# Kernel tuning notes

Hardware: AMD Instinct MI355X
Metric: run time of the kernel (lower is better)

## Reference

```python
import jax, jax.numpy as jnp
import numpy as np

B, T, C = 2, 2048, 512
H = 16
HS = C // H  # 32
DF = 4 * C   # 2048
EPS = 1e-3   # keras LayerNormalization default


def setup_inputs() -> dict:
    key = jax.random.key(0)
    ks = jax.random.split(key, 16)
    s = 0.02
    return {
        "x":  jax.random.normal(ks[0], (B, T, C), jnp.float32),
        "Wq": jax.random.normal(ks[1], (H, C, HS), jnp.float32) * s,
        "bq": jnp.zeros((H, HS), jnp.float32),
        "Wk": jax.random.normal(ks[2], (H, C, HS), jnp.float32) * s,
        "bk": jnp.zeros((H, HS), jnp.float32),
        "Wv": jax.random.normal(ks[3], (H, C, HS), jnp.float32) * s,
        "bv": jnp.zeros((H, HS), jnp.float32),
        "Wo": jax.random.normal(ks[4], (C, C), jnp.float32) * s,
        "bo": jnp.zeros((C,), jnp.float32),
        "W1": jax.random.normal(ks[5], (C, DF), jnp.float32) * s,
        "b1": jnp.zeros((DF,), jnp.float32),
        "W2": jax.random.normal(ks[6], (DF, C), jnp.float32) * s,
        "b2": jnp.zeros((C,), jnp.float32),
        "g1": jnp.ones((C,), jnp.float32),
        "be1": jnp.zeros((C,), jnp.float32),
        "g2": jnp.ones((C,), jnp.float32),
        "be2": jnp.zeros((C,), jnp.float32),
    }


def _layernorm(x, g, b):
    mu = jnp.mean(x, axis=-1, keepdims=True)
    var = jnp.mean(jnp.square(x - mu), axis=-1, keepdims=True)
    return (x - mu) / jnp.sqrt(var + EPS) * g + b


def reference(x, Wq, bq, Wk, bk, Wv, bv, Wo, bo, W1, b1, W2, b2, g1, be1, g2, be2):
    Bx, Tx, Cx = x.shape
    # --- attention branch (pre-LN) ---
    h = _layernorm(x, g1, be1)
    q = jnp.einsum('btc,hcd->bhtd', h, Wq) + bq[None, :, None, :]
    k = jnp.einsum('btc,hcd->bhtd', h, Wk) + bk[None, :, None, :]
    v = jnp.einsum('btc,hcd->bhtd', h, Wv) + bv[None, :, None, :]
    # NOTE: source code never applies 1/sqrt(head_size) to scores (mask-only scaling bug)
    scores = jnp.einsum('bhtd,bhsd->bhts', q, k)           # [B,H,T,T]
    causal = jnp.tril(jnp.ones((Tx, Tx), dtype=bool))
    scores = jnp.where(causal, scores, -jnp.inf)
    att = jax.nn.softmax(scores, axis=-1)
    o = jnp.einsum('bhts,bhsd->bhtd', att, v)              # [B,H,T,HS]
    o = o.transpose(0, 2, 1, 3).reshape(Bx, Tx, Cx)        # concat heads
    x = x + o @ Wo + bo
    # --- FFN branch (pre-LN) ---
    h2 = _layernorm(x, g2, be2)
    f = jax.nn.relu(h2 @ W1 + b1) @ W2 + b2
    return x + f
```

## Files before the change

### kernel.cpp

```cpp
#include <hip/hip_runtime.h>
#include <hip/hip_bf16.h>

#define T_  2048
#define C_  512
#define H_  16
#define HS_ 32
#define DF_ 2048
#define B_  2
#define M_  4096

typedef __attribute__((ext_vector_type(8))) short short8;
typedef __attribute__((ext_vector_type(4))) short short4v;
typedef __attribute__((ext_vector_type(4))) float f32x4;
typedef __attribute__((ext_vector_type(16))) float f32x16;

__device__ inline short bf16r(float f) {
  union { float f; unsigned u; } v; v.f = f;
  return (short)((v.u + 0x7FFFu + ((v.u >> 16) & 1u)) >> 16);
}

__device__ inline f32x4 mfma16(short8 a, short8 b, f32x4 c) {
  return __builtin_amdgcn_mfma_f32_16x16x32_bf16(a, b, c, 0, 0, 0);
}
__device__ inline f32x16 mfma32(short8 a, short8 b, f32x16 c) {
  return __builtin_amdgcn_mfma_f32_32x32x16_bf16(a, b, c, 0, 0, 0);
}

__device__ inline unsigned cvtpk(float lo, float hi) {
  unsigned r;
  asm("v_cvt_pk_bf16_f32 %0, %1, %2" : "=v"(r) : "v"(lo), "v"(hi));
  return r;
}

__device__ inline void gload_lds16(const short* g, short* l) {
  __builtin_amdgcn_global_load_lds(
      (const __attribute__((address_space(1))) unsigned int*)g,
      (__attribute__((address_space(3))) unsigned int*)l, 16, 0, 0);
}

__device__ inline void ln_row(int row, const float* src, const float* g,
                              const float* be, short* dst, int lane) {
  const float* xr = src + (size_t)row * C_;
  float4 a = *(const float4*)(xr + lane * 8);
  float4 b = *(const float4*)(xr + lane * 8 + 4);
  float vals[8] = {a.x, a.y, a.z, a.w, b.x, b.y, b.z, b.w};
  float s = 0.f, ss = 0.f;
  #pragma unroll
  for (int i = 0; i < 8; ++i) { s += vals[i]; ss += vals[i] * vals[i]; }
  #pragma unroll
  for (int off = 1; off < 64; off <<= 1) {
    s += __shfl_xor(s, off);
    ss += __shfl_xor(ss, off);
  }
  float mu = s * (1.f / C_);
  float rstd = rsqrtf(ss * (1.f / C_) - mu * mu + 1e-3f);
  short8 o;
  #pragma unroll
  for (int i = 0; i < 8; ++i)
    o[i] = bf16r((vals[i] - mu) * rstd * g[lane * 8 + i] + be[lane * 8 + i]);
  *(short8*)(dst + (size_t)row * C_ + lane * 8) = o;
}

__global__ __launch_bounds__(256) void prep_kernel(
    const float* __restrict__ x, const float* __restrict__ g1, const float* __restrict__ be1,
    const float* __restrict__ Wq, const float* __restrict__ Wk, const float* __restrict__ Wv,
    const float* __restrict__ Wo, const float* __restrict__ W1, const float* __restrict__ W2,
    short* __restrict__ h1, short* __restrict__ Wqkv, short* __restrict__ Wop,
    short* __restrict__ W1p, short* __restrict__ W2p) {
  __shared__ float tile[32][33];
  int id = blockIdx.x;
  int tid = threadIdx.x;
  if (id >= 3072) {
    int w = tid >> 6, lane = tid & 63;
    ln_row((id - 3072) * 4 + w, x, g1, be1, h1, lane);
    return;
  }
  const float* src; short* dst;
  int srcN, dstK, k0, n0;
  size_t dstBase;
  if (id < 768) {
    int s = id >> 4, ct = id & 15;
    int proj = s >> 4, hh = s & 15;
    src = (proj == 0 ? Wq : (proj == 1 ? Wk : Wv)) + (size_t)hh * 512 * 32;
    srcN = 32; dstK = 512; k0 = ct * 32; n0 = 0;
    dst = Wqkv; dstBase = (size_t)(proj * 512 + hh * 32);
  } else if (id < 1024) {
    int t = id - 768;
    src = Wo; srcN = 512; dstK = 512;
    k0 = (t >> 4) * 32; n0 = (t & 15) * 32; dst = Wop; dstBase = 0;
  } else if (id < 2048) {
    int t = id - 1024;
    src = W1; srcN = 2048; dstK = 512;
    k0 = (t >> 6) * 32; n0 = (t & 63) * 32; dst = W1p; dstBase = 0;
  } else {
    int t = id - 2048;
    src = W2; srcN = 512; dstK = 2048;
    k0 = (t >> 4) * 32; n0 = (t & 15) * 32; dst = W2p; dstBase = 0;
  }
  int rr = tid >> 3, rc = (tid & 7) * 4;
  float4 v4 = *(const float4*)(src + (size_t)(k0 + rr) * srcN + n0 + rc);
  tile[rr][rc + 0] = v4.x; tile[rr][rc + 1] = v4.y;
  tile[rr][rc + 2] = v4.z; tile[rr][rc + 3] = v4.w;
  __syncthreads();
  int wn = tid >> 3, wk = (tid & 7) * 4;
  short4v o;
  o[0] = bf16r(tile[wk + 0][wn]);
  o[1] = bf16r(tile[wk + 1][wn]);
  o[2] = bf16r(tile[wk + 2][wn]);
  o[3] = bf16r(tile[wk + 3][wn]);
  *(short4v*)(dst + (dstBase + n0 + wn) * (size_t)dstK + k0 + wk) = o;
}

__global__ __launch_bounds__(256) void ln2_kernel(
    const float* __restrict__ x, const float* __restrict__ g, const float* __restrict__ be,
    short* __restrict__ out) {
  int w = threadIdx.x >> 6, lane = threadIdx.x & 63;
  ln_row(blockIdx.x * 4 + w, x, g, be, out, lane);
}

template<int BM, int BN, int WM, int WN, int KDIM, int FM, int FN>
__device__ inline void gemm_core(const short* __restrict__ A, const short* __restrict__ Bw,
                                 int m0, int n0, f32x4 (&acc)[FM][FN]) {
  static_assert(WM * WN == 4 && FM == BM / WM / 16 && FN == BN / WN / 16, "geometry");
  __shared__ short lA[2][BM * 64];
  __shared__ short lB[2][BN * 64];
  const int tid = threadIdx.x, w = tid >> 6, lane = tid & 63;
  const int cl = lane & 15, g = lane >> 4;
  const int wm = w / WN, wn = w % WN;
  const int srow = tid >> 3;
  const int sug  = (tid & 7) ^ (srow & 7);
  constexpr int NT = KDIM / 64;

  auto stage = [&](int buf, int k0) {
    #pragma unroll
    for (int j = 0; j < BM / 32; ++j)
      gload_lds16(A + (size_t)(m0 + j * 32 + srow) * KDIM + k0 + sug * 8,
                  &lA[buf][j * 2048 + tid * 8]);
    #pragma unroll
    for (int j = 0; j < BN / 32; ++j)
      gload_lds16(Bw + (size_t)(n0 + j * 32 + srow) * KDIM + k0 + sug * 8,
                  &lB[buf][j * 2048 + tid * 8]);
  };

  stage(0, 0);
  __syncthreads();
  int cur = 0;
  for (int t = 0; t < NT; ++t) {
    if (t + 1 < NT) stage(cur ^ 1, (t + 1) * 64);
    #pragma unroll
    for (int kk = 0; kk < 2; ++kk) {
      const int uswz = ((kk * 4 + g) ^ (cl & 7)) * 8;
      short8 a[FM], b[FN];
      #pragma unroll
      for (int mi = 0; mi < FM; ++mi)
        a[mi] = *(const short8*)&lA[cur][(wm * (BM / WM) + mi * 16 + cl) * 64 + uswz];
      #pragma unroll
      for (int ni = 0; ni < FN; ++ni)
        b[ni] = *(const short8*)&lB[cur][(wn * (BN / WN) + ni * 16 + cl) * 64 + uswz];
      #pragma unroll
      for (int mi = 0; mi < FM; ++mi)
        #pragma unroll
        for (int ni = 0; ni < FN; ++ni)
          acc[mi][ni] = mfma16(a[mi], b[ni], acc[mi][ni]);
    }
    __syncthreads();
    cur ^= 1;
  }
}

__global__ __launch_bounds__(256) void gemm_qkvt(
    const short* __restrict__ h1, const short* __restrict__ Wqkv,
    const float* __restrict__ bq, const float* __restrict__ bk,
    const float* __restrict__ bv,
    short* __restrict__ qb, short* __restrict__ kb, short* __restrict__ vTb) {
  int id = blockIdx.x;
  const short *Ap, *Bp;
  int m0, n0;
  bool isv = id >= 256;
  if (!isv) {
    int xcd = id & 7, s = id >> 3;
    m0 = (xcd * 4 + (s & 3)) * 128;
    n0 = (s >> 2) * 128;
    Ap = h1; Bp = Wqkv;
  } else {
    int t = id - 256;
    int xcd = t & 7, s = t >> 3;
    n0 = (xcd * 4 + (s & 3)) * 128;
    m0 = (s >> 2) * 128;
    Ap = Wqkv + 1024 * 512; Bp = h1;
  }
  f32x4 acc[4][4] = {};
  gemm_core<128, 128, 2, 2, 512, 4, 4>(Ap, Bp, m0, n0, acc);
  int w = threadIdx.x >> 6, lane = threadIdx.x & 63;
  int cl = lane & 15, rb = (lane >> 4) * 4;
  int wm = w >> 1, wn = w & 1;
  if (!isv) {
    #pragma unroll
    for (int mi = 0; mi < 4; ++mi)
      #pragma unroll
      for (int ni = 0; ni < 4; ++ni)
        #pragma unroll
        for (int r = 0; r < 4; ++r) {
          int mm = m0 + wm * 64 + mi * 16 + rb + r;
          int n  = n0 + wn * 64 + ni * 16 + cl;
          int proj = n >> 9, rem = n & 511;
          int hh = rem >> 5, d = rem & 31;
          int b = mm >> 11, t = mm & (T_ - 1);
          size_t bh = (size_t)b * H_ + hh;
          float val = acc[mi][ni][r];
          if (proj == 0) qb[(bh * T_ + t) * HS_ + d] = bf16r(val + bq[rem]);
          else           kb[(bh * T_ + t) * HS_ + d] = bf16r(val + bk[rem]);
        }
  } else {
    #pragma unroll
    for (int mi = 0; mi < 4; ++mi)
      #pragma unroll
      for (int ni = 0; ni < 4; ++ni)
        #pragma unroll
        for (int r = 0; r < 4; ++r) {
          int m = m0 + wm * 64 + mi * 16 + rb + r;
          int n = n0 + wn * 64 + ni * 16 + cl;
          vTb[(size_t)(n >> 11) * (512 * 2048) + (size_t)m * T_ + (n & 2047)] =
              bf16r(acc[mi][ni][r] + bv[m]);
        }
  }
}

__global__ __launch_bounds__(256) void gemm_out(
    const short* __restrict__ A, const short* __restrict__ W,
    const float* __restrict__ bo, const float* __restrict__ xres,
    float* __restrict__ x1) {
  int id = blockIdx.x;
  int xcd = id & 7, s = id >> 3;
  int m0 = (xcd * 8 + (s & 7)) * 64;
  int n0 = (s >> 3) * 64;
  f32x4 acc[2][2] = {};
  gemm_core<64, 64, 2, 2, 512, 2, 2>(A, W, m0, n0, acc);
  int w = threadIdx.x >> 6, lane = threadIdx.x & 63;
  int cl = lane & 15, rb = (lane >> 4) * 4;
  int wm = w >> 1, wn = w & 1;
  #pragma unroll
  for (int mi = 0; mi < 2; ++mi)
    #pragma unroll
    for (int ni = 0; ni < 2; ++ni)
      #pragma unroll
      for (int r = 0; r < 4; ++r) {
        int mm = m0 + wm * 32 + mi * 16 + rb + r;
        int n  = n0 + wn * 32 + ni * 16 + cl;
        x1[(size_t)mm * C_ + n] = acc[mi][ni][r] + bo[n] + xres[(size_t)mm * C_ + n];
      }
}

__global__ __launch_bounds__(256) void gemm_ffn1(
    const short* __restrict__ A, const short* __restrict__ W,
    const float* __restrict__ b1, short* __restrict__ f1) {
  int id = blockIdx.x;
  int xcd = id & 7, s = id >> 3;
  int m0 = (xcd * 4 + (s & 3)) * 128;
  int n0 = (s >> 2) * 128;
  f32x4 acc[4][4] = {};
  gemm_core<128, 128, 2, 2, 512, 4, 4>(A, W, m0, n0, acc);
  int w = threadIdx.x >> 6, lane = threadIdx.x & 63;
  int cl = lane & 15, rb = (lane >> 4) * 4;
  int wm = w >> 1, wn = w & 1;
  #pragma unroll
  for (int mi = 0; mi < 4; ++mi)
    #pragma unroll
    for (int ni = 0; ni < 4; ++ni)
      #pragma unroll
      for (int r = 0; r < 4; ++r) {
        int mm = m0 + wm * 64 + mi * 16 + rb + r;
        int n  = n0 + wn * 64 + ni * 16 + cl;
        f1[(size_t)mm * DF_ + n] = bf16r(fmaxf(acc[mi][ni][r] + b1[n], 0.f));
      }
}

__global__ __launch_bounds__(256) void gemm_ffn2(
    const short* __restrict__ A, const short* __restrict__ W,
    const float* __restrict__ b2, const float* __restrict__ x1,
    float* __restrict__ out) {
  int id = blockIdx.x;
  int xcd = id & 7, s = id >> 3;
  int m0 = (xcd * 8 + (s & 7)) * 64;
  int n0 = (s >> 3) * 64;
  f32x4 acc[2][2] = {};
  gemm_core<64, 64, 2, 2, 2048, 2, 2>(A, W, m0, n0, acc);
  int w = threadIdx.x >> 6, lane = threadIdx.x & 63;
  int cl = lane & 15, rb = (lane >> 4) * 4;
  int wm = w >> 1, wn = w & 1;
  #pragma unroll
  for (int mi = 0; mi < 2; ++mi)
    #pragma unroll
    for (int ni = 0; ni < 2; ++ni)
      #pragma unroll
      for (int r = 0; r < 4; ++r) {
        int mm = m0 + wm * 32 + mi * 16 + rb + r;
        int n  = n0 + wn * 32 + ni * 16 + cl;
        out[(size_t)mm * C_ + n] = acc[mi][ni][r] + b2[n] + x1[(size_t)mm * C_ + n];
      }
}

__global__ __launch_bounds__(256) void attn_kernel(
    const short* __restrict__ qb, const short* __restrict__ kb,
    const short* __restrict__ vTb, short* __restrict__ ob) {
  __shared__ float accbuf[4][64][17];
  __shared__ float lbuf[4][32];
  __shared__ short tbuf[32][34];
  const int id = blockIdx.x;
  const int xcd = id & 7, s = id >> 3;
  const int headin = s & 3;
  const int qt = 63 - (s >> 2);
  const int bh = xcd * 4 + headin;
  const int w = threadIdx.x >> 6, lane = threadIdx.x & 63;
  const int cl = lane & 31, g = lane >> 5;
  const int q0 = qt * 32, q = q0 + cl;
  const float L2E = 1.44269504f;
  const float NFM = -16.f * L2E;

  const short* Qp  = qb  + (size_t)bh * T_ * HS_;
  const short* Kp  = kb  + (size_t)bh * T_ * HS_;
  const short* VTp = vTb + (size_t)bh * HS_ * T_;

  const int nc   = qt + 1;
  const int cbeg = (nc * w) >> 2;
  const int cend = (nc * (w + 1)) >> 2;

  f32x16 acc = {};
  float l = 0.f;

  if (cbeg < cend) {
    short8 qf0 = *(const short8*)(Qp + (size_t)q * HS_ + g * 8);
    short8 qf1 = *(const short8*)(Qp + (size_t)q * HS_ + 16 + g * 8);
    const int kc0 = cbeg << 5;
    short8 ka  = *(const short8*)(Kp + (size_t)(kc0 + cl) * HS_ + g * 8);
    short8 kc2 = *(const short8*)(Kp + (size_t)(kc0 + cl) * HS_ + 16 + g * 8);
    short8 va  = *(const short8*)(VTp + (size_t)cl * T_ + kc0 + g * 8);
    short8 vb  = *(const short8*)(VTp + (size_t)cl * T_ + kc0 + 16 + g * 8);

    for (int c = cbeg; c < cend; ++c) {
      const int kc = c << 5;
      f32x16 Z = {};
      f32x16 S = mfma32(ka, qf0, Z);
      S = mfma32(kc2, qf1, S);

      short8 kan, kbn, van, vbn;
      if (c + 1 < cend) {
        const int kn = kc + 32;
        kan = *(const short8*)(Kp + (size_t)(kn + cl) * HS_ + g * 8);
        kbn = *(const short8*)(Kp + (size_t)(kn + cl) * HS_ + 16 + g * 8);
        van = *(const short8*)(VTp + (size_t)cl * T_ + kn + g * 8);
        vbn = *(const short8*)(VTp + (size_t)cl * T_ + kn + 16 + g * 8);
      }

      if (c == nc - 1) {
        #pragma unroll
        for (int r = 0; r < 16; ++r) {
          int key = kc + (r & 3) + 8 * (r >> 2) + 4 * g;
          if (key > q) S[r] = -1e30f;
        }
      }

      float p[16];
      #pragma unroll
      for (int r = 0; r < 16; ++r) p[r] = exp2f(fmaf(S[r], L2E, NFM));
      float sm[8];
      #pragma unroll
      for (int r = 0; r < 8; ++r) sm[r] = p[r] + p[r + 8];
      #pragma unroll
      for (int r = 0; r < 4; ++r) sm[r] += sm[r + 4];
      float ps = (sm[0] + sm[1]) + (sm[2] + sm[3]);
      ps += __shfl_xor(ps, 32);
      l += ps;

      #pragma unroll
      for (int sb = 0; sb < 2; ++sb) {
        unsigned L0 = cvtpk(p[sb * 8 + 0], p[sb * 8 + 1]);
        unsigned L1 = cvtpk(p[sb * 8 + 2], p[sb * 8 + 3]);
        unsigned H0 = cvtpk(p[sb * 8 + 4], p[sb * 8 + 5]);
        unsigned H1 = cvtpk(p[sb * 8 + 6], p[sb * 8 + 7]);
        auto r02 = __builtin_amdgcn_permlane32_swap(L0, H0, false, false);
        auto r13 = __builtin_amdgcn_permlane32_swap(L1, H1, false, false);
        union { unsigned u[4]; short8 v; } pb;
        pb.u[0] = r02[0]; pb.u[1] = r13[0]; pb.u[2] = r02[1]; pb.u[3] = r13[1];
        acc = mfma32(sb == 0 ? va : vb, pb.v, acc);
      }

      ka = kan; kc2 = kbn; va = van; vb = vbn;
    }
  }

  #pragma unroll
  for (int r = 0; r < 16; ++r) accbuf[w][lane][r] = acc[r];
  if (lane < 32) lbuf[w][cl] = l;
  __syncthreads();

  if (w == 0) {
    float lsum = lbuf[0][cl] + lbuf[1][cl] + lbuf[2][cl] + lbuf[3][cl];
    float inv = 1.f / lsum;
    #pragma unroll
    for (int r = 0; r < 16; ++r) {
      float v = accbuf[0][lane][r] + accbuf[1][lane][r] +
                accbuf[2][lane][r] + accbuf[3][lane][r];
      int d = (r & 3) + 8 * (r >> 2) + 4 * g;
      tbuf[cl][d] = bf16r(v * inv);
    }
  }
  __syncthreads();

  int qr = threadIdx.x >> 3, col = (threadIdx.x & 7) * 4;
  const int b = bh >> 4, hh = bh & 15;
  short4v o4;
  o4[0] = tbuf[qr][col + 0];
  o4[1] = tbuf[qr][col + 1];
  o4[2] = tbuf[qr][col + 2];
  o4[3] = tbuf[qr][col + 3];
  *(short4v*)(ob + ((size_t)b * T_ + q0 + qr) * C_ + hh * HS_ + col) = o4;
}

#define OFF_H1   ((size_t)0)
#define OFF_WQKV ((size_t)4194304)
#define OFF_WO   ((size_t)5767168)
#define OFF_W1   ((size_t)6291456)
#define OFF_W2   ((size_t)8388608)
#define OFF_Q    ((size_t)10485760)
#define OFF_K    ((size_t)14680064)
#define OFF_VT   ((size_t)18874368)
#define OFF_O    ((size_t)23068672)
#define OFF_X1   ((size_t)27262976)
#define OFF_H2   ((size_t)35651584)
#define OFF_F1   ((size_t)39845888)

extern "C" void kernel_launch(void* const* d_in, const int* in_sizes, int n_in,
                              void* d_out, int out_size, void* d_ws, size_t ws_size,
                              hipStream_t stream) {
  const float* x   = (const float*)d_in[0];
  const float* Wq  = (const float*)d_in[1];
  const float* bq  = (const float*)d_in[2];
  const float* Wk  = (const float*)d_in[3];
  const float* bk  = (const float*)d_in[4];
  const float* Wv  = (const float*)d_in[5];
  const float* bv  = (const float*)d_in[6];
  const float* Wo  = (const float*)d_in[7];
  const float* bo  = (const float*)d_in[8];
  const float* W1  = (const float*)d_in[9];
  const float* b1  = (const float*)d_in[10];
  const float* W2  = (const float*)d_in[11];
  const float* b2  = (const float*)d_in[12];
  const float* g1  = (const float*)d_in[13];
  const float* be1 = (const float*)d_in[14];
  const float* g2  = (const float*)d_in[15];
  const float* be2 = (const float*)d_in[16];

  char* ws = (char*)d_ws;
  short* h1   = (short*)(ws + OFF_H1);
  short* Wqkv = (short*)(ws + OFF_WQKV);
  short* Wop  = (short*)(ws + OFF_WO);
  short* W1p  = (short*)(ws + OFF_W1);
  short* W2p  = (short*)(ws + OFF_W2);
  short* qb   = (short*)(ws + OFF_Q);
  short* kb   = (short*)(ws + OFF_K);
  short* vTb  = (short*)(ws + OFF_VT);
  short* ob   = (short*)(ws + OFF_O);
  float* x1   = (float*)(ws + OFF_X1);
  short* h2   = (short*)(ws + OFF_H2);
  short* f1   = (short*)(ws + OFF_F1);
  float* out  = (float*)d_out;

  prep_kernel<<<3072 + 1024, 256, 0, stream>>>(x, g1, be1, Wq, Wk, Wv, Wo, W1, W2,
                                               h1, Wqkv, Wop, W1p, W2p);
  gemm_qkvt<<<384, 256, 0, stream>>>(h1, Wqkv, bq, bk, bv, qb, kb, vTb);
  attn_kernel<<<2048, 256, 0, stream>>>(qb, kb, vTb, ob);
  gemm_out<<<512, 256, 0, stream>>>(ob, Wop, bo, x, x1);
  ln2_kernel<<<M_ / 4, 256, 0, stream>>>(x1, g2, be2, h2);
  gemm_ffn1<<<512, 256, 0, stream>>>(h2, W1p, b1, f1);
  gemm_ffn2<<<512, 256, 0, stream>>>(f1, W2p, b2, x1, out);
}
```

Measured before the change: 109.1 us.

## Process 64-key chunks in attention and retile QKV GEMM to 64x128

The attention inner loop now handles 64 keys per iteration with two independent score MFMAs and four PV MFMAs. This halves loop-iteration and reduction overhead per key and gives the scheduler more independent work. V fragments are now loaded at the top of each iteration instead of being prefetched, which may expose load latency. The QKV projection GEMM switches from 128x128 to 64x128 tiles, doubling the grid to 768 blocks for better CU occupancy, and drops the XCD-aware block swizzle.

Result: no change. 107.3 us (-1.7%).

```diff
diff --git a/kernel.cpp b/kernel.cpp
--- a/kernel.cpp
+++ b/kernel.cpp
@@ -176,32 +176,23 @@
   int id = blockIdx.x;
   const short *Ap, *Bp;
   int m0, n0;
-  bool isv = id >= 256;
-  if (!isv) {
-    int xcd = id & 7, s = id >> 3;
-    m0 = (xcd * 4 + (s & 3)) * 128;
-    n0 = (s >> 2) * 128;
-    Ap = h1; Bp = Wqkv;
-  } else {
-    int t = id - 256;
-    int xcd = t & 7, s = t >> 3;
-    n0 = (xcd * 4 + (s & 3)) * 128;
-    m0 = (s >> 2) * 128;
-    Ap = Wqkv + 1024 * 512; Bp = h1;
-  }
-  f32x4 acc[4][4] = {};
-  gemm_core<128, 128, 2, 2, 512, 4, 4>(Ap, Bp, m0, n0, acc);
+  bool isv = id >= 512;
+  if (!isv) { m0 = (id >> 3) * 64; n0 = (id & 7) * 128; Ap = h1; Bp = Wqkv; }
+  else { int t = id - 512; m0 = (t & 7) * 64; n0 = (t >> 3) * 128;
+         Ap = Wqkv + 1024 * 512; Bp = h1; }
+  f32x4 acc[2][4] = {};
+  gemm_core<64, 128, 2, 2, 512, 2, 4>(Ap, Bp, m0, n0, acc);
   int w = threadIdx.x >> 6, lane = threadIdx.x & 63;
   int cl = lane & 15, rb = (lane >> 4) * 4;
   int wm = w >> 1, wn = w & 1;
   if (!isv) {
     #pragma unroll
-    for (int mi = 0; mi < 4; ++mi)
+    for (int mi = 0; mi < 2; ++mi)
       #pragma unroll
       for (int ni = 0; ni < 4; ++ni)
         #pragma unroll
         for (int r = 0; r < 4; ++r) {
-          int mm = m0 + wm * 64 + mi * 16 + rb + r;
+          int mm = m0 + wm * 32 + mi * 16 + rb + r;
           int n  = n0 + wn * 64 + ni * 16 + cl;
           int proj = n >> 9, rem = n & 511;
           int hh = rem >> 5, d = rem & 31;
@@ -213,12 +204,12 @@
         }
   } else {
     #pragma unroll
-    for (int mi = 0; mi < 4; ++mi)
+    for (int mi = 0; mi < 2; ++mi)
       #pragma unroll
       for (int ni = 0; ni < 4; ++ni)
         #pragma unroll
         for (int r = 0; r < 4; ++r) {
-          int m = m0 + wm * 64 + mi * 16 + rb + r;
+          int m = m0 + wm * 32 + mi * 16 + rb + r;
           int n = n0 + wn * 64 + ni * 16 + cl;
           vTb[(size_t)(n >> 11) * (512 * 2048) + (size_t)m * T_ + (n & 2047)] =
               bf16r(acc[mi][ni][r] + bv[m]);
@@ -321,7 +312,7 @@
   const short* Kp  = kb  + (size_t)bh * T_ * HS_;
   const short* VTp = vTb + (size_t)bh * HS_ * T_;
 
-  const int nc   = qt + 1;
+  const int nc   = (qt >> 1) + 1;
   const int cbeg = (nc * w) >> 2;
   const int cend = (nc * (w + 1)) >> 2;
 
@@ -331,41 +322,52 @@
   if (cbeg < cend) {
     short8 qf0 = *(const short8*)(Qp + (size_t)q * HS_ + g * 8);
     short8 qf1 = *(const short8*)(Qp + (size_t)q * HS_ + 16 + g * 8);
-    const int kc0 = cbeg << 5;
-    short8 ka  = *(const short8*)(Kp + (size_t)(kc0 + cl) * HS_ + g * 8);
-    short8 kc2 = *(const short8*)(Kp + (size_t)(kc0 + cl) * HS_ + 16 + g * 8);
-    short8 va  = *(const short8*)(VTp + (size_t)cl * T_ + kc0 + g * 8);
-    short8 vb  = *(const short8*)(VTp + (size_t)cl * T_ + kc0 + 16 + g * 8);
+    const int kc0 = cbeg << 6;
+    short8 k00 = *(const short8*)(Kp + (size_t)(kc0 + cl) * HS_ + g * 8);
+    short8 k01 = *(const short8*)(Kp + (size_t)(kc0 + cl) * HS_ + 16 + g * 8);
+    short8 k10 = *(const short8*)(Kp + (size_t)(kc0 + 32 + cl) * HS_ + g * 8);
+    short8 k11 = *(const short8*)(Kp + (size_t)(kc0 + 32 + cl) * HS_ + 16 + g * 8);
 
     for (int c = cbeg; c < cend; ++c) {
-      const int kc = c << 5;
+      const int kc = c << 6;
+      short8 va = *(const short8*)(VTp + (size_t)cl * T_ + kc + g * 8);
+      short8 vb = *(const short8*)(VTp + (size_t)cl * T_ + kc + 16 + g * 8);
+      short8 vc = *(const short8*)(VTp + (size_t)cl * T_ + kc + 32 + g * 8);
+      short8 vd = *(const short8*)(VTp + (size_t)cl * T_ + kc + 48 + g * 8);
+
       f32x16 Z = {};
-      f32x16 S = mfma32(ka, qf0, Z);
-      S = mfma32(kc2, qf1, S);
-
-      short8 kan, kbn, van, vbn;
+      f32x16 S0 = mfma32(k00, qf0, Z);
+      S0 = mfma32(k01, qf1, S0);
+      f32x16 S1 = mfma32(k10, qf0, Z);
+      S1 = mfma32(k11, qf1, S1);
+
       if (c + 1 < cend) {
-        const int kn = kc + 32;
-        kan = *(const short8*)(Kp + (size_t)(kn + cl) * HS_ + g * 8);
-        kbn = *(const short8*)(Kp + (size_t)(kn + cl) * HS_ + 16 + g * 8);
-        van = *(const short8*)(VTp + (size_t)cl * T_ + kn + g * 8);
-        vbn = *(const short8*)(VTp + (size_t)cl * T_ + kn + 16 + g * 8);
+        const int kn = kc + 64;
+        k00 = *(const short8*)(Kp + (size_t)(kn + cl) * HS_ + g * 8);
+        k01 = *(const short8*)(Kp + (size_t)(kn + cl) * HS_ + 16 + g * 8);
+        k10 = *(const short8*)(Kp + (size_t)(kn + 32 + cl) * HS_ + g * 8);
+        k11 = *(const short8*)(Kp + (size_t)(kn + 32 + cl) * HS_ + 16 + g * 8);
       }
 
       if (c == nc - 1) {
         #pragma unroll
         for (int r = 0; r < 16; ++r) {
           int key = kc + (r & 3) + 8 * (r >> 2) + 4 * g;
-          if (key > q) S[r] = -1e30f;
+          if (key > q)      S0[r] = -1e30f;
+          if (key + 32 > q) S1[r] = -1e30f;
         }
       }
 
-      float p[16];
-      #pragma unroll
-      for (int r = 0; r < 16; ++r) p[r] = exp2f(fmaf(S[r], L2E, NFM));
+      float p[32];
+      #pragma unroll
+      for (int r = 0; r < 16; ++r) {
+        p[r]      = exp2f(fmaf(S0[r], L2E, NFM));
+        p[16 + r] = exp2f(fmaf(S1[r], L2E, NFM));
+      }
       float sm[8];
       #pragma unroll
-      for (int r = 0; r < 8; ++r) sm[r] = p[r] + p[r + 8];
+      for (int r = 0; r < 8; ++r)
+        sm[r] = (p[r] + p[r + 8]) + (p[16 + r] + p[24 + r]);
       #pragma unroll
       for (int r = 0; r < 4; ++r) sm[r] += sm[r + 4];
       float ps = (sm[0] + sm[1]) + (sm[2] + sm[3]);
@@ -373,7 +375,7 @@
       l += ps;
 
       #pragma unroll
-      for (int sb = 0; sb < 2; ++sb) {
+      for (int sb = 0; sb < 4; ++sb) {
         unsigned L0 = cvtpk(p[sb * 8 + 0], p[sb * 8 + 1]);
         unsigned L1 = cvtpk(p[sb * 8 + 2], p[sb * 8 + 3]);
         unsigned H0 = cvtpk(p[sb * 8 + 4], p[sb * 8 + 5]);
@@ -382,10 +384,9 @@
         auto r13 = __builtin_amdgcn_permlane32_swap(L1, H1, false, false);
         union { unsigned u[4]; short8 v; } pb;
         pb.u[0] = r02[0]; pb.u[1] = r13[0]; pb.u[2] = r02[1]; pb.u[3] = r13[1];
-        acc = mfma32(sb == 0 ? va : vb, pb.v, acc);
-      }
-
-      ka = kan; kc2 = kbn; va = van; vb = vbn;
+        short8 vf = (sb == 0) ? va : (sb == 1) ? vb : (sb == 2) ? vc : vd;
+        acc = mfma32(vf, pb.v, acc);
+      }
     }
   }
 
@@ -468,7 +469,7 @@
 
   prep_kernel<<<3072 + 1024, 256, 0, stream>>>(x, g1, be1, Wq, Wk, Wv, Wo, W1, W2,
                                                h1, Wqkv, Wop, W1p, W2p);
-  gemm_qkvt<<<384, 256, 0, stream>>>(h1, Wqkv, bq, bk, bv, qb, kb, vTb);
+  gemm_qkvt<<<768, 256, 0, stream>>>(h1, Wqkv, bq, bk, bv, qb, kb, vTb);
   attn_kernel<<<2048, 256, 0, stream>>>(qb, kb, vTb, ob);
   gemm_out<<<512, 256, 0, stream>>>(ob, Wop, bo, x, x1);
   ln2_kernel<<<M_ / 4, 256, 0, stream>>>(x1, g2, be2, h2);
```
